# Optimization experiments

Hardware: AMD Instinct MI355X
Metric: run time of the kernel (lower is better)

## Reference

```python
import jax, jax.numpy as jnp
import numpy as np

BATCH, IN_DIM, LATENT, K = 16384, 768, 12288, 32

def setup_inputs() -> dict:
    key = jax.random.key(0)
    k1, k2, k3 = jax.random.split(key, 3)
    # kaiming-uniform-style scale for encoder/decoder weights
    enc_bound = float(np.sqrt(6.0 / IN_DIM))
    dec_bound = float(np.sqrt(6.0 / LATENT))
    x = jax.random.normal(k1, (BATCH, IN_DIM), dtype=jnp.float32)
    enc_w = jax.random.uniform(k2, (LATENT, IN_DIM), dtype=jnp.float32, minval=-enc_bound, maxval=enc_bound)
    enc_b = jnp.zeros((LATENT,), dtype=jnp.float32)
    dec_w = jax.random.uniform(k3, (IN_DIM, LATENT), dtype=jnp.float32, minval=-dec_bound, maxval=dec_bound)
    dec_b = jnp.zeros((IN_DIM,), dtype=jnp.float32)
    return {"x": x, "enc_w": enc_w, "enc_b": enc_b, "dec_w": dec_w, "dec_b": dec_b, "k": K}

def reference(x, enc_w, enc_b, dec_w, dec_b, k):
    # encode: z = x @ W_e^T + b_e            [B, LATENT]
    z = jnp.einsum('bi,li->bl', x, enc_w) + enc_b
    # top-k threshold: kth largest value per row, then shifted relu
    vals, _ = jax.lax.top_k(z, k)
    thresh = vals[:, -1:]                     # [B, 1]
    z_sparse = jax.nn.relu(z - thresh)
    # decode: dense GEMM over all latent columns (as in original module)
    x_recon = jnp.einsum('bl,il->bi', z_sparse, dec_w) + dec_b
    return (x_recon, z_sparse)
```

## Files before the change

### kernel.cpp

```cpp
#include <hip/hip_runtime.h>

#define M_DIM 16384
#define K_DIM 768
#define N_DIM 12288
#define TOPK  32
#define NCHUNK (N_DIM / 128)

typedef float f32x4 __attribute__((ext_vector_type(4)));
typedef short s16x8 __attribute__((ext_vector_type(8)));

__device__ __forceinline__ unsigned f2u(float f) {
  union { float f; unsigned u; } v; v.f = f; return v.u;
}
__device__ __forceinline__ float u2f(unsigned u) {
  union { unsigned u; float f; } v; v.u = u; return v.f;
}
__device__ __forceinline__ unsigned fkey(float f) {
  const unsigned u = f2u(f);
  return u ^ (unsigned)(((int)u >> 31) | 0x80000000);
}
__device__ __forceinline__ float kinv(unsigned k) {
  return u2f((k & 0x80000000u) ? (k ^ 0x80000000u) : ~k);
}
__device__ __forceinline__ unsigned short bf16_rne(float f) {
  unsigned u = f2u(f);
  return (unsigned short)((u + 0x7FFFu + ((u >> 16) & 1u)) >> 16);
}

__global__ __launch_bounds__(256) void TopKSparseAutoencoder_51917564674099_prep(
    const float* __restrict__ x, const float* __restrict__ w,
    const float* __restrict__ dw,
    unsigned short* __restrict__ xhi, unsigned short* __restrict__ xlo,
    unsigned short* __restrict__ whi, unsigned short* __restrict__ wlo,
    float* __restrict__ WT, int do_t, int do_s)
{
  __shared__ float tile[32][33];
  const int b = (int)blockIdx.x;
  const int t = (int)threadIdx.x;

  if (b < 9216) {
    if (!do_t) return;
    const int bx = b % (N_DIM / 32);
    const int by = b / (N_DIM / 32);
    const int tx = t & 31, ty = t >> 5;
#pragma unroll
    for (int j = 0; j < 32; j += 8)
      tile[ty + j][tx] = dw[(size_t)(by * 32 + ty + j) * N_DIM + bx * 32 + tx];
    __syncthreads();
#pragma unroll
    for (int j = 0; j < 32; j += 8)
      WT[(size_t)(bx * 32 + ty + j) * K_DIM + by * 32 + tx] = tile[tx][ty + j];
    return;
  }
  if (!do_s) return;

  const float* src; unsigned short* dh; unsigned short* dl; int i, stride, n4;
  if (b < 9216 + 1024) {
    src = x; dh = xhi; dl = xlo;
    i = (b - 9216) * 256 + t; stride = 1024 * 256; n4 = M_DIM * K_DIM / 4;
  } else {
    src = w; dh = whi; dl = wlo;
    i = (b - 10240) * 256 + t; stride = 512 * 256; n4 = N_DIM * K_DIM / 4;
  }
  for (; i < n4; i += stride) {
    const float4 v = ((const float4*)src)[i];
    ushort4 h, l;
    h.x = bf16_rne(v.x); h.y = bf16_rne(v.y); h.z = bf16_rne(v.z); h.w = bf16_rne(v.w);
    l.x = bf16_rne(v.x - u2f((unsigned)h.x << 16));
    l.y = bf16_rne(v.y - u2f((unsigned)h.y << 16));
    l.z = bf16_rne(v.z - u2f((unsigned)h.z << 16));
    l.w = bf16_rne(v.w - u2f((unsigned)h.w << 16));
    ((ushort4*)dh)[i] = h;
    ((ushort4*)dl)[i] = l;
  }
}

__device__ __forceinline__ void mfma16(f32x4& d, s16x8 a, s16x8 b) {
  asm("v_mfma_f32_16x16x32_bf16 %0, %1, %2, %0" : "+v"(d) : "v"(a), "v"(b));
}

#define GL16(g, l) __builtin_amdgcn_global_load_lds(                      \
    (const __attribute__((address_space(1))) void*)(g),                   \
    (__attribute__((address_space(3))) void*)(l), 16, 0, 0)

__global__ __launch_bounds__(256, 2) void TopKSparseAutoencoder_51917564674099_kernel(
    const unsigned short* __restrict__ Ahi, const unsigned short* __restrict__ Alo,
    const unsigned short* __restrict__ Bhi, const unsigned short* __restrict__ Blo,
    const float* __restrict__ bias, float* __restrict__ Z,
    float* __restrict__ cmax, int do_cmax)
{
  __shared__ unsigned short lds[4][128][32];
  __shared__ float cmx[128][2];

  const int t    = (int)threadIdx.x;
  const int wid  = t >> 6;
  const int lane = t & 63;

  const int bid  = (int)(blockIdx.y * gridDim.x + blockIdx.x);
  const int bswz = (bid & 7) * (12288 / 8) + (bid >> 3);
  const int n0   = (bswz % 96) * 128;
  const int m0   = (bswz / 96) * 128;

  const int rr  = lane >> 2;
  const int kq  = lane & 3;
  const int rt0 = wid * 32 + rr;
  const int rt1 = rt0 + 16;
  const int kc0 = (kq ^ ((rt0 >> 1) & 3)) * 8;
  const int kc1 = (kq ^ ((rt1 >> 1) & 3)) * 8;
  const size_t offA0 = (size_t)(m0 + rt0) * K_DIM + kc0;
  const size_t offA1 = (size_t)(m0 + rt1) * K_DIM + kc1;
  const size_t offB0 = (size_t)(n0 + rt0) * K_DIM + kc0;
  const size_t offB1 = (size_t)(n0 + rt1) * K_DIM + kc1;

  const int wm = (wid >> 1) * 64;
  const int wn = (wid & 1) * 64;
  const int lr = lane & 15;
  const int lc = lane >> 4;

  f32x4 acc[4][4];
#pragma unroll
  for (int i = 0; i < 4; ++i)
#pragma unroll
    for (int j = 0; j < 4; ++j) acc[i][j] = (f32x4){0.f, 0.f, 0.f, 0.f};

  for (int k0 = 0; k0 < K_DIM; k0 += 32) {
    GL16(Ahi + offA0 + k0, &lds[0][wid * 32][0]);
    GL16(Ahi + offA1 + k0, &lds[0][wid * 32 + 16][0]);
    GL16(Alo + offA0 + k0, &lds[1][wid * 32][0]);
    GL16(Alo + offA1 + k0, &lds[1][wid * 32 + 16][0]);
    GL16(Bhi + offB0 + k0, &lds[2][wid * 32][0]);
    GL16(Bhi + offB1 + k0, &lds[2][wid * 32 + 16][0]);
    GL16(Blo + offB0 + k0, &lds[3][wid * 32][0]);
    GL16(Blo + offB1 + k0, &lds[3][wid * 32 + 16][0]);
    __syncthreads();

    s16x8 ah[4], al[4], bh[4], bl[4];
#pragma unroll
    for (int i = 0; i < 4; ++i) {
      const int r = wm + i * 16 + lr;
      const int p = (lc ^ ((r >> 1) & 3)) * 8;
      ah[i] = *(const s16x8*)&lds[0][r][p];
      al[i] = *(const s16x8*)&lds[1][r][p];
    }
#pragma unroll
    for (int j = 0; j < 4; ++j) {
      const int r = wn + j * 16 + lr;
      const int p = (lc ^ ((r >> 1) & 3)) * 8;
      bh[j] = *(const s16x8*)&lds[2][r][p];
      bl[j] = *(const s16x8*)&lds[3][r][p];
    }
#pragma unroll
    for (int i = 0; i < 4; ++i)
#pragma unroll
      for (int j = 0; j < 4; ++j) {
        mfma16(acc[i][j], ah[i], bh[j]);
        mfma16(acc[i][j], ah[i], bl[j]);
        mfma16(acc[i][j], al[i], bh[j]);
      }
    __syncthreads();
  }

  asm volatile("s_nop 7\n\ts_nop 7" :::);

  float mx[4][4];
#pragma unroll
  for (int i = 0; i < 4; ++i)
#pragma unroll
    for (int q = 0; q < 4; ++q) mx[i][q] = -3.4e38f;

#pragma unroll
  for (int j = 0; j < 4; ++j) {
    const int col = n0 + wn + j * 16 + lr;
    const float bb = bias[col];
#pragma unroll
    for (int i = 0; i < 4; ++i) {
      const int r0 = m0 + wm + i * 16 + lc * 4;
#pragma unroll
      for (int q = 0; q < 4; ++q) {
        const float val = acc[i][j][q] + bb;
        Z[(size_t)(r0 + q) * N_DIM + col] = val;
        mx[i][q] = fmaxf(mx[i][q], val);
      }
    }
  }

  if (do_cmax) {
#pragma unroll
    for (int s = 1; s < 16; s <<= 1)
#pragma unroll
      for (int i = 0; i < 4; ++i)
#pragma unroll
        for (int q = 0; q < 4; ++q)
          mx[i][q] = fmaxf(mx[i][q], __shfl_xor(mx[i][q], s));
    if (lr == 0) {
#pragma unroll
      for (int i = 0; i < 4; ++i)
#pragma unroll
        for (int q = 0; q < 4; ++q)
          cmx[wm + i * 16 + lc * 4 + q][wid & 1] = mx[i][q];
    }
    __syncthreads();
    if (t < 128)
      cmax[(size_t)(m0 + t) * NCHUNK + (n0 >> 7)] = fmaxf(cmx[t][0], cmx[t][1]);
  }
}

__global__ void enc_gemm_f32_fb(
    const float* A, const float* B, const float* bias, float* Z)
{
  __shared__ float As[32][132];
  __shared__ float Bs[32][132];

  const int tx = (int)threadIdx.x;
  const int ty = (int)threadIdx.y;
  const int t  = ty * 16 + tx;
  const int n0 = (int)blockIdx.x * 128;
  const int m0 = (int)blockIdx.y * 128;
  const int r = t >> 1;
  const int h = (t & 1) * 16;

  float c[8][8];
#pragma unroll
  for (int i = 0; i < 8; ++i)
#pragma unroll
    for (int j = 0; j < 8; ++j) c[i][j] = 0.0f;

  for (int k0 = 0; k0 < K_DIM; k0 += 32) {
    const float* pa = A + (size_t)(m0 + r) * K_DIM + k0 + h;
    const float* pb = B + (size_t)(n0 + r) * K_DIM + k0 + h;
    float fa[16], fb[16];
#pragma unroll
    for (int j = 0; j < 16; ++j) fa[j] = pa[j];
#pragma unroll
    for (int j = 0; j < 16; ++j) fb[j] = pb[j];
#pragma unroll
    for (int j = 0; j < 16; ++j) As[h + j][r] = fa[j];
#pragma unroll
    for (int j = 0; j < 16; ++j) Bs[h + j][r] = fb[j];
    __syncthreads();

    for (int kk = 0; kk < 32; ++kk) {
      float av[8], bv[8];
#pragma unroll
      for (int i = 0; i < 8; ++i) av[i] = As[kk][ty * 8 + i];
#pragma unroll
      for (int j = 0; j < 8; ++j) bv[j] = Bs[kk][tx * 8 + j];
#pragma unroll
      for (int i = 0; i < 8; ++i)
#pragma unroll
        for (int j = 0; j < 8; ++j) c[i][j] += av[i] * bv[j];
    }
    __syncthreads();
  }

#pragma unroll
  for (int j = 0; j < 8; ++j) {
    const int col = n0 + tx * 8 + j;
    const float bb = bias[col];
#pragma unroll
    for (int i = 0; i < 8; ++i)
      Z[(size_t)(m0 + ty * 8 + i) * N_DIM + col] = c[i][j] + bb;
  }
}

__global__ __launch_bounds__(256, 4) void TopKSparseAutoencoder_51917564674099_zdecode(
    float* Z, const float* __restrict__ CMAX, const float* __restrict__ WT,
    const float* __restrict__ db, float* __restrict__ XR)
{
  __shared__ unsigned candk[512];
  __shared__ int      candi[512];
  __shared__ unsigned red[2][2][4];
  __shared__ unsigned s_B;
  __shared__ int s_cc, s_nnz;
  __shared__ int   s_col[TOPK];
  __shared__ float s_val[TOPK];

  const int row  = (int)blockIdx.x;
  const int t    = (int)threadIdx.x;
  const int lane = t & 63;
  const int wid  = t >> 6;

  if (t == 0) { s_cc = 0; s_nnz = 0; }
  if (t < TOPK) { s_col[t] = 0; s_val[t] = 0.0f; }

  if (wid == 0) {
    const unsigned kA = fkey(CMAX[(size_t)row * NCHUNK + lane]);
    const unsigned kB = (lane < NCHUNK - 64) ? fkey(CMAX[(size_t)row * NCHUNK + 64 + lane]) : 0u;
    unsigned lo = 0;
    unsigned long long w = 1ULL << 32;
    for (int r = 0; r < 8; ++r) {
      w >>= 2;
      const unsigned wu = (unsigned)w;
      const unsigned m1 = lo + wu, m2 = lo + 2u * wu, m3 = lo + 3u * wu;
      unsigned p = (unsigned)((kA >= m1) + (kB >= m1)) |
                   ((unsigned)((kA >= m2) + (kB >= m2)) << 16);
      unsigned q = (unsigned)((kA >= m3) + (kB >= m3));
      p += __shfl_down(p, 32); q += __shfl_down(q, 32);
      p += __shfl_down(p, 16); q += __shfl_down(q, 16);
      p += __shfl_down(p, 8);  q += __shfl_down(q, 8);
      p += __shfl_down(p, 4);  q += __shfl_down(q, 4);
      p += __shfl_down(p, 2);  q += __shfl_down(q, 2);
      p += __shfl_down(p, 1);  q += __shfl_down(q, 1);
      p = __shfl(p, 0); q = __shfl(q, 0);
      if (q >= (unsigned)TOPK)                  lo = m3;
      else if ((p >> 16) >= (unsigned)TOPK)     lo = m2;
      else if ((p & 0xFFFFu) >= (unsigned)TOPK) lo = m1;
    }
    if (lane == 0) s_B = lo;
  }
  __syncthreads();
  const unsigned B = s_B;

  const float4* zr = (const float4*)(Z + (size_t)row * N_DIM);
#pragma unroll
  for (int j = 0; j < 12; ++j) {
    const float4 v = zr[t + 256 * j];
    const int base = (t + 256 * j) * 4;
    const unsigned k0 = fkey(v.x), k1 = fkey(v.y), k2 = fkey(v.z), k3 = fkey(v.w);
    if (k0 >= B) { int p = atomicAdd(&s_cc, 1); if (p < 512) { candk[p] = k0; candi[p] = base; } }
    if (k1 >= B) { int p = atomicAdd(&s_cc, 1); if (p < 512) { candk[p] = k1; candi[p] = base + 1; } }
    if (k2 >= B) { int p = atomicAdd(&s_cc, 1); if (p < 512) { candk[p] = k2; candi[p] = base + 2; } }
    if (k3 >= B) { int p = atomicAdd(&s_cc, 1); if (p < 512) { candk[p] = k3; candi[p] = base + 3; } }
  }
  __syncthreads();
  const int cc = s_cc;
  float4* zw = (float4*)(Z + (size_t)row * N_DIM);

  if (cc <= 512) {
    if (wid == 0) {
      unsigned k[8];
#pragma unroll
      for (int i = 0; i < 8; ++i) k[i] = (lane + 64 * i < cc) ? candk[lane + 64 * i] : 0u;
      unsigned lo = 0;
      unsigned long long w = 1ULL << 32;
      for (int r = 0; r < 16; ++r) {
        w >>= 2;
        const unsigned wu = (unsigned)w;
        const unsigned m1 = lo + wu, m2 = lo + 2u * wu, m3 = lo + 3u * wu;
        unsigned c1 = 0, c2 = 0, c3 = 0;
#pragma unroll
        for (int i = 0; i < 8; ++i) {
          c1 += (k[i] >= m1); c2 += (k[i] >= m2); c3 += (k[i] >= m3);
        }
        unsigned p = c1 | (c2 << 16), q = c3;
        p += __shfl_down(p, 32); q += __shfl_down(q, 32);
        p += __shfl_down(p, 16); q += __shfl_down(q, 16);
        p += __shfl_down(p, 8);  q += __shfl_down(q, 8);
        p += __shfl_down(p, 4);  q += __shfl_down(q, 4);
        p += __shfl_down(p, 2);  q += __shfl_down(q, 2);
        p += __shfl_down(p, 1);  q += __shfl_down(q, 1);
        p = __shfl(p, 0); q = __shfl(q, 0);
        if (q >= (unsigned)TOPK)                  lo = m3;
        else if ((p >> 16) >= (unsigned)TOPK)     lo = m2;
        else if ((p & 0xFFFFu) >= (unsigned)TOPK) lo = m1;
      }
      const unsigned T = lo;
      const float thresh = kinv(T);
      for (int i = lane; i < cc; i += 64) {
        const unsigned ck = candk[i];
        if (ck > T) {
          const int p = atomicAdd(&s_nnz, 1);
          if (p < TOPK) { s_col[p] = candi[i]; s_val[p] = kinv(ck) - thresh; }
        }
      }
    } else {
      const float4 z4 = {0.f, 0.f, 0.f, 0.f};
#pragma unroll
      for (int jj = 0; jj < 16; ++jj)
        zw[(wid - 1) * 64 + lane + 192 * jj] = z4;
    }
    __syncthreads();
  } else {
    unsigned lo = 0;
    unsigned long long w = 1ULL << 32;
    for (int r = 0; r < 16; ++r) {
      w >>= 2;
      const unsigned wu = (unsigned)w;
      const unsigned m1 = lo + wu, m2 = lo + 2u * wu, m3 = lo + 3u * wu;
      unsigned c1 = 0, c2 = 0, c3 = 0;
      for (int j = 0; j < 12; ++j) {
        const float4 v = zr[t + 256 * j];
        const unsigned k0 = fkey(v.x), k1 = fkey(v.y), k2 = fkey(v.z), k3 = fkey(v.w);
        c1 += (k0 >= m1) + (k1 >= m1) + (k2 >= m1) + (k3 >= m1);
        c2 += (k0 >= m2) + (k1 >= m2) + (k2 >= m2) + (k3 >= m2);
        c3 += (k0 >= m3) + (k1 >= m3) + (k2 >= m3) + (k3 >= m3);
      }
      unsigned p = c1 | (c2 << 16), q = c3;
      p += __shfl_down(p, 32); q += __shfl_down(q, 32);
      p += __shfl_down(p, 16); q += __shfl_down(q, 16);
      p += __shfl_down(p, 8);  q += __shfl_down(q, 8);
      p += __shfl_down(p, 4);  q += __shfl_down(q, 4);
      p += __shfl_down(p, 2);  q += __shfl_down(q, 2);
      p += __shfl_down(p, 1);  q += __shfl_down(q, 1);
      const int par = r & 1;
      if (lane == 0) { red[par][0][wid] = p; red[par][1][wid] = q; }
      __syncthreads();
      const unsigned P = red[par][0][0] + red[par][0][1] + red[par][0][2] + red[par][0][3];
      const unsigned Q = red[par][1][0] + red[par][1][1] + red[par][1][2] + red[par][1][3];
      if (Q >= (unsigned)TOPK)                  lo = m3;
      else if ((P >> 16) >= (unsigned)TOPK)     lo = m2;
      else if ((P & 0xFFFFu) >= (unsigned)TOPK) lo = m1;
    }
    const unsigned T = lo;
    const float thresh = kinv(T);
    const float4 z4 = {0.f, 0.f, 0.f, 0.f};
    for (int j = 0; j < 12; ++j) {
      const float4 v = zr[t + 256 * j];
      const int base = (t + 256 * j) * 4;
      const unsigned k0 = fkey(v.x), k1 = fkey(v.y), k2 = fkey(v.z), k3 = fkey(v.w);
      if (k0 > T) { int p = atomicAdd(&s_nnz, 1); if (p < TOPK) { s_col[p] = base;     s_val[p] = kinv(k0) - thresh; } }
      if (k1 > T) { int p = atomicAdd(&s_nnz, 1); if (p < TOPK) { s_col[p] = base + 1; s_val[p] = kinv(k1) - thresh; } }
      if (k2 > T) { int p = atomicAdd(&s_nnz, 1); if (p < TOPK) { s_col[p] = base + 2; s_val[p] = kinv(k2) - thresh; } }
      if (k3 > T) { int p = atomicAdd(&s_nnz, 1); if (p < TOPK) { s_col[p] = base + 3; s_val[p] = kinv(k3) - thresh; } }
      zw[t + 256 * j] = z4;
    }
    __syncthreads();
  }

  const int nnz = (s_nnz < TOPK) ? s_nnz : TOPK;
  if (t < nnz) Z[(size_t)row * N_DIM + s_col[t]] = s_val[t];

  float a0 = 0.0f, a1 = 0.0f, a2 = 0.0f;
#pragma unroll 8
  for (int j = 0; j < TOPK; ++j) {
    const float v = s_val[j];
    const float* wp = WT + (size_t)s_col[j] * K_DIM;
    a0 += v * wp[t];
    a1 += v * wp[t + 256];
    a2 += v * wp[t + 512];
  }
  float* xr = XR + (size_t)row * K_DIM;
  xr[t]       = a0 + db[t];
  xr[t + 256] = a1 + db[t + 256];
  xr[t + 512] = a2 + db[t + 512];
}

__device__ __forceinline__ void full_round_l(
    const uint4* zk, unsigned red[][2][4], int t, int lane, int wid, int r,
    unsigned& lo, unsigned long long& w)
{
  w >>= 2;
  const unsigned wu = (unsigned)w;
  const unsigned m1 = lo + wu, m2 = lo + 2u * wu, m3 = lo + 3u * wu;
  unsigned c1 = 0, c2 = 0, c3 = 0;
#pragma unroll
  for (int j = 0; j < 12; ++j) {
    const uint4 k = zk[t + 256 * j];
    c1 += (k.x >= m1) + (k.y >= m1) + (k.z >= m1) + (k.w >= m1);
    c2 += (k.x >= m2) + (k.y >= m2) + (k.z >= m2) + (k.w >= m2);
    c3 += (k.x >= m3) + (k.y >= m3) + (k.z >= m3) + (k.w >= m3);
  }
  unsigned p = c1 | (c2 << 16), q = c3;
  p += __shfl_down(p, 32); q += __shfl_down(q, 32);
  p += __shfl_down(p, 16); q += __shfl_down(q, 16);
  p += __shfl_down(p, 8);  q += __shfl_down(q, 8);
  p += __shfl_down(p, 4);  q += __shfl_down(q, 4);
  p += __shfl_down(p, 2);  q += __shfl_down(q, 2);
  p += __shfl_down(p, 1);  q += __shfl_down(q, 1);
  const int par = r & 1;
  if (lane == 0) { red[par][0][wid] = p; red[par][1][wid] = q; }
  __syncthreads();
  const unsigned P = red[par][0][0] + red[par][0][1] + red[par][0][2] + red[par][0][3];
  const unsigned Q = red[par][1][0] + red[par][1][1] + red[par][1][2] + red[par][1][3];
  if (Q >= (unsigned)TOPK)                lo = m3;
  else if ((P >> 16) >= (unsigned)TOPK)   lo = m2;
  else if ((P & 0xFFFFu) >= (unsigned)TOPK) lo = m1;
}

__global__ __launch_bounds__(256, 3) void topk_select_decode_fb(
    float* Z, const float* __restrict__ WT, const float* __restrict__ DW,
    const float* __restrict__ db, float* __restrict__ XR, int use_wt)
{
  __shared__ uint4 zkey4[N_DIM / 4];
  __shared__ unsigned red[2][2][4];
  __shared__ unsigned cand[256];
  __shared__ unsigned s_T;
  __shared__ int s_cc;
  __shared__ int s_nnz;
  __shared__ int   s_col[TOPK];
  __shared__ float s_val[TOPK];

  const int row  = (int)blockIdx.x;
  const int t    = (int)threadIdx.x;
  const int lane = t & 63;
  const int wid  = t >> 6;

  float4* zv = (float4*)(Z + (size_t)row * N_DIM);

#pragma unroll
  for (int j = 0; j < 12; ++j) {
    const float4 v = zv[t + 256 * j];
    uint4 k;
    k.x = fkey(v.x); k.y = fkey(v.y); k.z = fkey(v.z); k.w = fkey(v.w);
    zkey4[t + 256 * j] = k;
  }
  if (t == 0) { s_nnz = 0; s_cc = 0; }
  if (t < TOPK) { s_col[t] = 0; s_val[t] = 0.0f; }
  __syncthreads();

  unsigned lo = 0;
  unsigned long long w = 1ULL << 32;
  for (int r = 0; r < 8; ++r)
    full_round_l(zkey4, red, t, lane, wid, r, lo, w);

#pragma unroll
  for (int j = 0; j < 12; ++j) {
    const uint4 k = zkey4[t + 256 * j];
    if (k.x >= lo) { int p = atomicAdd(&s_cc, 1); if (p < 256) cand[p] = k.x; }
    if (k.y >= lo) { int p = atomicAdd(&s_cc, 1); if (p < 256) cand[p] = k.y; }
    if (k.z >= lo) { int p = atomicAdd(&s_cc, 1); if (p < 256) cand[p] = k.z; }
    if (k.w >= lo) { int p = atomicAdd(&s_cc, 1); if (p < 256) cand[p] = k.w; }
  }
  __syncthreads();
  const int cc = s_cc;

  if (cc <= 256) {
    if (wid == 0) {
      const unsigned k0 = (lane       < cc) ? cand[lane]       : 0u;
      const unsigned k1 = (lane + 64  < cc) ? cand[lane + 64]  : 0u;
      const unsigned k2 = (lane + 128 < cc) ? cand[lane + 128] : 0u;
      const unsigned k3 = (lane + 192 < cc) ? cand[lane + 192] : 0u;
      for (int r = 8; r < 16; ++r) {
        w >>= 2;
        const unsigned wu = (unsigned)w;
        const unsigned m1 = lo + wu, m2 = lo + 2u * wu, m3 = lo + 3u * wu;
        unsigned c1 = (k0 >= m1) + (k1 >= m1) + (k2 >= m1) + (k3 >= m1);
        unsigned c2 = (k0 >= m2) + (k1 >= m2) + (k2 >= m2) + (k3 >= m2);
        unsigned c3 = (k0 >= m3) + (k1 >= m3) + (k2 >= m3) + (k3 >= m3);
        unsigned p = c1 | (c2 << 16), q = c3;
        p += __shfl_down(p, 32); q += __shfl_down(q, 32);
        p += __shfl_down(p, 16); q += __shfl_down(q, 16);
        p += __shfl_down(p, 8);  q += __shfl_down(q, 8);
        p += __shfl_down(p, 4);  q += __shfl_down(q, 4);
        p += __shfl_down(p, 2);  q += __shfl_down(q, 2);
        p += __shfl_down(p, 1);  q += __shfl_down(q, 1);
        p = __shfl(p, 0); q = __shfl(q, 0);
        if (q >= (unsigned)TOPK)                  lo = m3;
        else if ((p >> 16) >= (unsigned)TOPK)     lo = m2;
        else if ((p & 0xFFFFu) >= (unsigned)TOPK) lo = m1;
      }
      if (lane == 0) s_T = lo;
    }
  } else {
    for (int r = 8; r < 16; ++r)
      full_round_l(zkey4, red, t, lane, wid, r, lo, w);
    if (t == 0) s_T = lo;
  }
  __syncthreads();
  const unsigned T = s_T;
  const float thresh = kinv(T);

#define COMPF(KF, OFS, OF) {                                                  \
      float v = 0.0f;                                                         \
      if (KF > T) {                                                           \
        v = kinv(KF) - thresh;                                                \
        const int p = atomicAdd(&s_nnz, 1);                                   \
        if (p < TOPK) { s_col[p] = base + OFS; s_val[p] = v; }                \
      }                                                                       \
      o.OF = v; }
#pragma unroll
  for (int j = 0; j < 12; ++j) {
    const uint4 k = zkey4[t + 256 * j];
    const int base = (t + 256 * j) * 4;
    float4 o;
    COMPF(k.x, 0, x)
    COMPF(k.y, 1, y)
    COMPF(k.z, 2, z)
    COMPF(k.w, 3, w)
    zv[t + 256 * j] = o;
  }
#undef COMPF
  __syncthreads();

  float a0 = 0.0f, a1 = 0.0f, a2 = 0.0f;
  if (use_wt) {
#pragma unroll 8
    for (int j = 0; j < TOPK; ++j) {
      const float v = s_val[j];
      const float* wp = WT + (size_t)s_col[j] * K_DIM;
      a0 += v * wp[t];
      a1 += v * wp[t + 256];
      a2 += v * wp[t + 512];
    }
  } else {
#pragma unroll 8
    for (int j = 0; j < TOPK; ++j) {
      const float v = s_val[j];
      const int col = s_col[j];
      a0 += v * DW[(size_t)(t)       * N_DIM + col];
      a1 += v * DW[(size_t)(t + 256) * N_DIM + col];
      a2 += v * DW[(size_t)(t + 512) * N_DIM + col];
    }
  }
  float* xr = XR + (size_t)row * K_DIM;
  xr[t]       = a0 + db[t];
  xr[t + 256] = a1 + db[t + 256];
  xr[t + 512] = a2 + db[t + 512];
}

extern "C" void kernel_launch(void* const* d_in, const int* in_sizes, int n_in,
                              void* d_out, int out_size, void* d_ws, size_t ws_size,
                              hipStream_t stream)
{
  (void)in_sizes; (void)n_in; (void)out_size;

  const float* x     = (const float*)d_in[0];
  const float* enc_w = (const float*)d_in[1];
  const float* enc_b = (const float*)d_in[2];
  const float* dec_w = (const float*)d_in[3];
  const float* dec_b = (const float*)d_in[4];

  float* out     = (float*)d_out;
  float* x_recon = out;
  float* z_sp    = out + (size_t)M_DIM * K_DIM;

  const size_t WT_BYTES = (size_t)N_DIM * K_DIM * sizeof(float);
  const size_t XPLANE   = (size_t)M_DIM * K_DIM * sizeof(unsigned short);
  const size_t WPLANE   = (size_t)N_DIM * K_DIM * sizeof(unsigned short);
  const size_t FULL     = WT_BYTES + 2 * XPLANE + 2 * WPLANE;
  const size_t CMAX_B   = (size_t)M_DIM * NCHUNK * sizeof(float);
  const size_t FULL2    = FULL + CMAX_B;

  char* ws = (char*)d_ws;
  const int use_wt   = (ws_size >= WT_BYTES) ? 1 : 0;
  const int use_mfma = (ws_size >= FULL) ? 1 : 0;
  const int use_cmax = (ws_size >= FULL2) ? 1 : 0;

  float*          WT   = (float*)ws;
  unsigned short* xhi  = (unsigned short*)(ws + WT_BYTES);
  unsigned short* xlo  = (unsigned short*)(ws + WT_BYTES + XPLANE);
  unsigned short* whi  = (unsigned short*)(ws + WT_BYTES + 2 * XPLANE);
  unsigned short* wlo  = (unsigned short*)(ws + WT_BYTES + 2 * XPLANE + WPLANE);
  float*          CMAX = (float*)(ws + FULL);

  if (use_wt || use_mfma)
    TopKSparseAutoencoder_51917564674099_prep<<<10752, 256, 0, stream>>>(
        x, enc_w, dec_w, xhi, xlo, whi, wlo, WT, use_wt, use_mfma);

  if (use_mfma) {
    dim3 tg(N_DIM / 128, M_DIM / 128);
    TopKSparseAutoencoder_51917564674099_kernel<<<tg, 256, 0, stream>>>(
        xhi, xlo, whi, wlo, enc_b, z_sp, CMAX, use_cmax);
  } else {
    dim3 tb(16, 16);
    dim3 tg(N_DIM / 128, M_DIM / 128);
    enc_gemm_f32_fb<<<tg, tb, 0, stream>>>(x, enc_w, enc_b, z_sp);
  }

  if (use_cmax)
    TopKSparseAutoencoder_51917564674099_zdecode<<<M_DIM, 256, 0, stream>>>(
        z_sp, CMAX, WT, dec_b, x_recon);
  else
    topk_select_decode_fb<<<M_DIM, 256, 0, stream>>>(
        z_sp, WT, dec_w, dec_b, x_recon, use_wt);
}
```

Baseline: 2.232 ms.

## Double-buffer GEMM LDS loads and scan only eligible chunks in top-k

The encoder GEMM now uses two LDS buffers: it prefetches the next K-slice with global_load_lds while MFMAs run on the current one, which removes one barrier per iteration. The top-k candidate pass now reads only the 128-column chunks whose max reaches the threshold, done by wave 0, instead of streaming the whole Z row across all 256 threads. LDS per GEMM block doubles, which may cut occupancy from 2 blocks/CU. The candidate scan becomes single-wave, and the zdecode launch-bounds hint is loosened. The prefetch issued before the compute reads is protected only by the trailing barrier, so ordering depends on the async LDS writes finishing correctly.

New measurement: 2.249 ms. Within noise of the previous version (+0.8%).

```diff
diff --git a/kernel.cpp b/kernel.cpp
--- a/kernel.cpp
+++ b/kernel.cpp
@@ -89,7 +89,7 @@
     const float* __restrict__ bias, float* __restrict__ Z,
     float* __restrict__ cmax, int do_cmax)
 {
-  __shared__ unsigned short lds[4][128][32];
+  __shared__ unsigned short lds[2][4][128][32];
   __shared__ float cmx[128][2];
 
   const int t    = (int)threadIdx.x;
@@ -123,31 +123,38 @@
 #pragma unroll
     for (int j = 0; j < 4; ++j) acc[i][j] = (f32x4){0.f, 0.f, 0.f, 0.f};
 
+#define STAGE(B, KOFF) do {                                          \
+    GL16(Ahi + offA0 + (KOFF), &lds[B][0][wid * 32][0]);             \
+    GL16(Ahi + offA1 + (KOFF), &lds[B][0][wid * 32 + 16][0]);        \
+    GL16(Alo + offA0 + (KOFF), &lds[B][1][wid * 32][0]);             \
+    GL16(Alo + offA1 + (KOFF), &lds[B][1][wid * 32 + 16][0]);        \
+    GL16(Bhi + offB0 + (KOFF), &lds[B][2][wid * 32][0]);             \
+    GL16(Bhi + offB1 + (KOFF), &lds[B][2][wid * 32 + 16][0]);        \
+    GL16(Blo + offB0 + (KOFF), &lds[B][3][wid * 32][0]);             \
+    GL16(Blo + offB1 + (KOFF), &lds[B][3][wid * 32 + 16][0]);        \
+  } while (0)
+
+  STAGE(0, 0);
+  __syncthreads();
+
+  int cur = 0;
   for (int k0 = 0; k0 < K_DIM; k0 += 32) {
-    GL16(Ahi + offA0 + k0, &lds[0][wid * 32][0]);
-    GL16(Ahi + offA1 + k0, &lds[0][wid * 32 + 16][0]);
-    GL16(Alo + offA0 + k0, &lds[1][wid * 32][0]);
-    GL16(Alo + offA1 + k0, &lds[1][wid * 32 + 16][0]);
-    GL16(Bhi + offB0 + k0, &lds[2][wid * 32][0]);
-    GL16(Bhi + offB1 + k0, &lds[2][wid * 32 + 16][0]);
-    GL16(Blo + offB0 + k0, &lds[3][wid * 32][0]);
-    GL16(Blo + offB1 + k0, &lds[3][wid * 32 + 16][0]);
-    __syncthreads();
+    if (k0 + 32 < K_DIM) STAGE(cur ^ 1, k0 + 32);
 
     s16x8 ah[4], al[4], bh[4], bl[4];
 #pragma unroll
     for (int i = 0; i < 4; ++i) {
       const int r = wm + i * 16 + lr;
       const int p = (lc ^ ((r >> 1) & 3)) * 8;
-      ah[i] = *(const s16x8*)&lds[0][r][p];
-      al[i] = *(const s16x8*)&lds[1][r][p];
+      ah[i] = *(const s16x8*)&lds[cur][0][r][p];
+      al[i] = *(const s16x8*)&lds[cur][1][r][p];
     }
 #pragma unroll
     for (int j = 0; j < 4; ++j) {
       const int r = wn + j * 16 + lr;
       const int p = (lc ^ ((r >> 1) & 3)) * 8;
-      bh[j] = *(const s16x8*)&lds[2][r][p];
-      bl[j] = *(const s16x8*)&lds[3][r][p];
+      bh[j] = *(const s16x8*)&lds[cur][2][r][p];
+      bl[j] = *(const s16x8*)&lds[cur][3][r][p];
     }
 #pragma unroll
     for (int i = 0; i < 4; ++i)
@@ -158,7 +165,9 @@
         mfma16(acc[i][j], al[i], bh[j]);
       }
     __syncthreads();
-  }
+    cur ^= 1;
+  }
+#undef STAGE
 
   asm volatile("s_nop 7\n\ts_nop 7" :::);
 
@@ -263,15 +272,15 @@
   }
 }
 
-__global__ __launch_bounds__(256, 4) void TopKSparseAutoencoder_51917564674099_zdecode(
+__global__ __launch_bounds__(256) void TopKSparseAutoencoder_51917564674099_zdecode(
     float* Z, const float* __restrict__ CMAX, const float* __restrict__ WT,
     const float* __restrict__ db, float* __restrict__ XR)
 {
   __shared__ unsigned candk[512];
   __shared__ int      candi[512];
+  __shared__ int      s_elig[NCHUNK];
   __shared__ unsigned red[2][2][4];
-  __shared__ unsigned s_B;
-  __shared__ int s_cc, s_nnz;
+  __shared__ int s_ne, s_cc, s_nnz;
   __shared__ int   s_col[TOPK];
   __shared__ float s_val[TOPK];
 
@@ -280,12 +289,15 @@
   const int lane = t & 63;
   const int wid  = t >> 6;
 
-  if (t == 0) { s_cc = 0; s_nnz = 0; }
+  if (t == 0) { s_ne = 0; s_cc = 0; s_nnz = 0; }
   if (t < TOPK) { s_col[t] = 0; s_val[t] = 0.0f; }
+
+  const float4* zr = (const float4*)(Z + (size_t)row * N_DIM);
 
   if (wid == 0) {
     const unsigned kA = fkey(CMAX[(size_t)row * NCHUNK + lane]);
     const unsigned kB = (lane < NCHUNK - 64) ? fkey(CMAX[(size_t)row * NCHUNK + 64 + lane]) : 0u;
+
     unsigned lo = 0;
     unsigned long long w = 1ULL << 32;
     for (int r = 0; r < 8; ++r) {
@@ -306,21 +318,22 @@
       else if ((p >> 16) >= (unsigned)TOPK)     lo = m2;
       else if ((p & 0xFFFFu) >= (unsigned)TOPK) lo = m1;
     }
-    if (lane == 0) s_B = lo;
-  }
-  __syncthreads();
-  const unsigned B = s_B;
-
-  const float4* zr = (const float4*)(Z + (size_t)row * N_DIM);
-#pragma unroll
-  for (int j = 0; j < 12; ++j) {
-    const float4 v = zr[t + 256 * j];
-    const int base = (t + 256 * j) * 4;
-    const unsigned k0 = fkey(v.x), k1 = fkey(v.y), k2 = fkey(v.z), k3 = fkey(v.w);
-    if (k0 >= B) { int p = atomicAdd(&s_cc, 1); if (p < 512) { candk[p] = k0; candi[p] = base; } }
-    if (k1 >= B) { int p = atomicAdd(&s_cc, 1); if (p < 512) { candk[p] = k1; candi[p] = base + 1; } }
-    if (k2 >= B) { int p = atomicAdd(&s_cc, 1); if (p < 512) { candk[p] = k2; candi[p] = base + 2; } }
-    if (k3 >= B) { int p = atomicAdd(&s_cc, 1); if (p < 512) { candk[p] = k3; candi[p] = base + 3; } }
+    const unsigned B = lo;
+
+    if (kA >= B) { const int p = atomicAdd(&s_ne, 1); s_elig[p] = lane; }
+    if (lane < NCHUNK - 64 && kB >= B) { const int p = atomicAdd(&s_ne, 1); s_elig[p] = lane + 64; }
+    const int ne = __shfl(s_ne, 0);
+    for (int i = (lane >> 5); i < ne; i += 2) {
+      const int c  = s_elig[i];
+      const int f4 = (c << 5) + (lane & 31);
+      const float4 v = zr[f4];
+      const int base = f4 << 2;
+      const unsigned k0 = fkey(v.x), k1 = fkey(v.y), k2 = fkey(v.z), k3 = fkey(v.w);
+      if (k0 >= B) { int p = atomicAdd(&s_cc, 1); if (p < 512) { candk[p] = k0; candi[p] = base; } }
+      if (k1 >= B) { int p = atomicAdd(&s_cc, 1); if (p < 512) { candk[p] = k1; candi[p] = base + 1; } }
+      if (k2 >= B) { int p = atomicAdd(&s_cc, 1); if (p < 512) { candk[p] = k2; candi[p] = base + 2; } }
+      if (k3 >= B) { int p = atomicAdd(&s_cc, 1); if (p < 512) { candk[p] = k3; candi[p] = base + 3; } }
+    }
   }
   __syncthreads();
   const int cc = s_cc;
```

## Process one row per wavefront and scan only eligible chunks in top-k decode

Applied to the files above, without the earlier changes.

The top-k/decode kernel now maps one row to each 64-lane wavefront (four rows per block) instead of one row per block, which removes the block-wide barriers. Using the per-chunk maxima, each wave collects the chunks whose max reaches the coarse bound and rereads only those 128-column chunks of Z to gather candidates, rather than scanning the whole row. The decode gather switches to 16-byte vector loads of WT rows, and a vmcnt wait orders the zeroing stores before the sparse value writes. The trade-off is less parallelism per row: each wave issues all 48 zeroing stores for its row, and the fallback path now does its full-row counting passes on a single wave.

Result: faster. 2.170 ms (-2.8%).

```diff
diff --git a/kernel.cpp b/kernel.cpp
--- a/kernel.cpp
+++ b/kernel.cpp
@@ -267,34 +267,84 @@
     float* Z, const float* __restrict__ CMAX, const float* __restrict__ WT,
     const float* __restrict__ db, float* __restrict__ XR)
 {
-  __shared__ unsigned candk[512];
-  __shared__ int      candi[512];
-  __shared__ unsigned red[2][2][4];
-  __shared__ unsigned s_B;
-  __shared__ int s_cc, s_nnz;
-  __shared__ int   s_col[TOPK];
-  __shared__ float s_val[TOPK];
-
-  const int row  = (int)blockIdx.x;
+  __shared__ unsigned candk[4][256];
+  __shared__ int      candi[4][256];
+  __shared__ short    s_elig[4][NCHUNK];
+  __shared__ int s_ne[4], s_cc[4], s_nnz[4];
+  __shared__ int   s_col[4][TOPK];
+  __shared__ float s_val[4][TOPK];
+
   const int t    = (int)threadIdx.x;
   const int lane = t & 63;
   const int wid  = t >> 6;
-
-  if (t == 0) { s_cc = 0; s_nnz = 0; }
-  if (t < TOPK) { s_col[t] = 0; s_val[t] = 0.0f; }
-
-  if (wid == 0) {
-    const unsigned kA = fkey(CMAX[(size_t)row * NCHUNK + lane]);
-    const unsigned kB = (lane < NCHUNK - 64) ? fkey(CMAX[(size_t)row * NCHUNK + 64 + lane]) : 0u;
-    unsigned lo = 0;
-    unsigned long long w = 1ULL << 32;
-    for (int r = 0; r < 8; ++r) {
+  const int row  = (int)blockIdx.x * 4 + wid;
+
+  if (lane == 0) { s_ne[wid] = 0; s_cc[wid] = 0; s_nnz[wid] = 0; }
+  if (lane < TOPK) { s_col[wid][lane] = 0; s_val[wid][lane] = 0.0f; }
+
+  const f32x4* zr = (const f32x4*)(Z + (size_t)row * N_DIM);
+  f32x4*       zw = (f32x4*)(Z + (size_t)row * N_DIM);
+
+  const unsigned kA = fkey(CMAX[(size_t)row * NCHUNK + lane]);
+  const unsigned kB = (lane < NCHUNK - 64) ? fkey(CMAX[(size_t)row * NCHUNK + 64 + lane]) : 0u;
+  unsigned lo = 0;
+  unsigned long long w = 1ULL << 32;
+  for (int r = 0; r < 8; ++r) {
+    w >>= 2;
+    const unsigned wu = (unsigned)w;
+    const unsigned m1 = lo + wu, m2 = lo + 2u * wu, m3 = lo + 3u * wu;
+    unsigned p = (unsigned)((kA >= m1) + (kB >= m1)) |
+                 ((unsigned)((kA >= m2) + (kB >= m2)) << 16);
+    unsigned q = (unsigned)((kA >= m3) + (kB >= m3));
+    p += __shfl_down(p, 32); q += __shfl_down(q, 32);
+    p += __shfl_down(p, 16); q += __shfl_down(q, 16);
+    p += __shfl_down(p, 8);  q += __shfl_down(q, 8);
+    p += __shfl_down(p, 4);  q += __shfl_down(q, 4);
+    p += __shfl_down(p, 2);  q += __shfl_down(q, 2);
+    p += __shfl_down(p, 1);  q += __shfl_down(q, 1);
+    p = __shfl(p, 0); q = __shfl(q, 0);
+    if (q >= (unsigned)TOPK)                  lo = m3;
+    else if ((p >> 16) >= (unsigned)TOPK)     lo = m2;
+    else if ((p & 0xFFFFu) >= (unsigned)TOPK) lo = m1;
+  }
+  const unsigned B = lo;
+
+  if (kA >= B) { const int p = atomicAdd(&s_ne[wid], 1); s_elig[wid][p] = (short)lane; }
+  if (lane < NCHUNK - 64 && kB >= B) {
+    const int p = atomicAdd(&s_ne[wid], 1); s_elig[wid][p] = (short)(lane + 64);
+  }
+  const int ne = s_ne[wid];
+
+  for (int i = (lane >> 5); i < ne; i += 2) {
+    const int c  = (int)s_elig[wid][i];
+    const int f4 = (c << 5) + (lane & 31);
+    const f32x4 v = zr[f4];
+    const int base = f4 << 2;
+    const unsigned k0 = fkey(v[0]), k1 = fkey(v[1]), k2 = fkey(v[2]), k3 = fkey(v[3]);
+    if (k0 >= B) { int p = atomicAdd(&s_cc[wid], 1); if (p < 256) { candk[wid][p] = k0; candi[wid][p] = base; } }
+    if (k1 >= B) { int p = atomicAdd(&s_cc[wid], 1); if (p < 256) { candk[wid][p] = k1; candi[wid][p] = base + 1; } }
+    if (k2 >= B) { int p = atomicAdd(&s_cc[wid], 1); if (p < 256) { candk[wid][p] = k2; candi[wid][p] = base + 2; } }
+    if (k3 >= B) { int p = atomicAdd(&s_cc[wid], 1); if (p < 256) { candk[wid][p] = k3; candi[wid][p] = base + 3; } }
+  }
+  const int cc = s_cc[wid];
+  const f32x4 z4 = (f32x4){0.f, 0.f, 0.f, 0.f};
+
+  if (cc <= 256) {
+#pragma unroll 8
+    for (int jj = 0; jj < 48; ++jj) zw[lane + 64 * jj] = z4;
+
+    unsigned k[4];
+#pragma unroll
+    for (int i = 0; i < 4; ++i) k[i] = (lane + 64 * i < cc) ? candk[wid][lane + 64 * i] : 0u;
+    lo = 0; w = 1ULL << 32;
+    for (int r = 0; r < 16; ++r) {
       w >>= 2;
       const unsigned wu = (unsigned)w;
       const unsigned m1 = lo + wu, m2 = lo + 2u * wu, m3 = lo + 3u * wu;
-      unsigned p = (unsigned)((kA >= m1) + (kB >= m1)) |
-                   ((unsigned)((kA >= m2) + (kB >= m2)) << 16);
-      unsigned q = (unsigned)((kA >= m3) + (kB >= m3));
+      unsigned c1 = 0, c2 = 0, c3 = 0;
+#pragma unroll
+      for (int i = 0; i < 4; ++i) { c1 += (k[i] >= m1); c2 += (k[i] >= m2); c3 += (k[i] >= m3); }
+      unsigned p = c1 | (c2 << 16), q = c3;
       p += __shfl_down(p, 32); q += __shfl_down(q, 32);
       p += __shfl_down(p, 16); q += __shfl_down(q, 16);
       p += __shfl_down(p, 8);  q += __shfl_down(q, 8);
@@ -306,81 +356,25 @@
       else if ((p >> 16) >= (unsigned)TOPK)     lo = m2;
       else if ((p & 0xFFFFu) >= (unsigned)TOPK) lo = m1;
     }
-    if (lane == 0) s_B = lo;
-  }
-  __syncthreads();
-  const unsigned B = s_B;
-
-  const float4* zr = (const float4*)(Z + (size_t)row * N_DIM);
-#pragma unroll
-  for (int j = 0; j < 12; ++j) {
-    const float4 v = zr[t + 256 * j];
-    const int base = (t + 256 * j) * 4;
-    const unsigned k0 = fkey(v.x), k1 = fkey(v.y), k2 = fkey(v.z), k3 = fkey(v.w);
-    if (k0 >= B) { int p = atomicAdd(&s_cc, 1); if (p < 512) { candk[p] = k0; candi[p] = base; } }
-    if (k1 >= B) { int p = atomicAdd(&s_cc, 1); if (p < 512) { candk[p] = k1; candi[p] = base + 1; } }
-    if (k2 >= B) { int p = atomicAdd(&s_cc, 1); if (p < 512) { candk[p] = k2; candi[p] = base + 2; } }
-    if (k3 >= B) { int p = atomicAdd(&s_cc, 1); if (p < 512) { candk[p] = k3; candi[p] = base + 3; } }
-  }
-  __syncthreads();
-  const int cc = s_cc;
-  float4* zw = (float4*)(Z + (size_t)row * N_DIM);
-
-  if (cc <= 512) {
-    if (wid == 0) {
-      unsigned k[8];
-#pragma unroll
-      for (int i = 0; i < 8; ++i) k[i] = (lane + 64 * i < cc) ? candk[lane + 64 * i] : 0u;
-      unsigned lo = 0;
-      unsigned long long w = 1ULL << 32;
-      for (int r = 0; r < 16; ++r) {
-        w >>= 2;
-        const unsigned wu = (unsigned)w;
-        const unsigned m1 = lo + wu, m2 = lo + 2u * wu, m3 = lo + 3u * wu;
-        unsigned c1 = 0, c2 = 0, c3 = 0;
-#pragma unroll
-        for (int i = 0; i < 8; ++i) {
-          c1 += (k[i] >= m1); c2 += (k[i] >= m2); c3 += (k[i] >= m3);
-        }
-        unsigned p = c1 | (c2 << 16), q = c3;
-        p += __shfl_down(p, 32); q += __shfl_down(q, 32);
-        p += __shfl_down(p, 16); q += __shfl_down(q, 16);
-        p += __shfl_down(p, 8);  q += __shfl_down(q, 8);
-        p += __shfl_down(p, 4);  q += __shfl_down(q, 4);
-        p += __shfl_down(p, 2);  q += __shfl_down(q, 2);
-        p += __shfl_down(p, 1);  q += __shfl_down(q, 1);
-        p = __shfl(p, 0); q = __shfl(q, 0);
-        if (q >= (unsigned)TOPK)                  lo = m3;
-        else if ((p >> 16) >= (unsigned)TOPK)     lo = m2;
-        else if ((p & 0xFFFFu) >= (unsigned)TOPK) lo = m1;
+    const unsigned T = lo;
+    const float thresh = kinv(T);
+    for (int i = lane; i < cc; i += 64) {
+      const unsigned ck = candk[wid][i];
+      if (ck > T) {
+        const int p = atomicAdd(&s_nnz[wid], 1);
+        if (p < TOPK) { s_col[wid][p] = candi[wid][i]; s_val[wid][p] = kinv(ck) - thresh; }
       }
-      const unsigned T = lo;
-      const float thresh = kinv(T);
-      for (int i = lane; i < cc; i += 64) {
-        const unsigned ck = candk[i];
-        if (ck > T) {
-          const int p = atomicAdd(&s_nnz, 1);
-          if (p < TOPK) { s_col[p] = candi[i]; s_val[p] = kinv(ck) - thresh; }
-        }
-      }
-    } else {
-      const float4 z4 = {0.f, 0.f, 0.f, 0.f};
-#pragma unroll
-      for (int jj = 0; jj < 16; ++jj)
-        zw[(wid - 1) * 64 + lane + 192 * jj] = z4;
-    }
-    __syncthreads();
+    }
   } else {
-    unsigned lo = 0;
-    unsigned long long w = 1ULL << 32;
+    lo = 0; w = 1ULL << 32;
     for (int r = 0; r < 16; ++r) {
       w >>= 2;
       const unsigned wu = (unsigned)w;
       const unsigned m1 = lo + wu, m2 = lo + 2u * wu, m3 = lo + 3u * wu;
       unsigned c1 = 0, c2 = 0, c3 = 0;
-      for (int j = 0; j < 12; ++j) {
-        const float4 v = zr[t + 256 * j];
-        const unsigned k0 = fkey(v.x), k1 = fkey(v.y), k2 = fkey(v.z), k3 = fkey(v.w);
+      for (int j = 0; j < 48; ++j) {
+        const f32x4 v = zr[lane + 64 * j];
+        const unsigned k0 = fkey(v[0]), k1 = fkey(v[1]), k2 = fkey(v[2]), k3 = fkey(v[3]);
         c1 += (k0 >= m1) + (k1 >= m1) + (k2 >= m1) + (k3 >= m1);
         c2 += (k0 >= m2) + (k1 >= m2) + (k2 >= m2) + (k3 >= m2);
         c3 += (k0 >= m3) + (k1 >= m3) + (k2 >= m3) + (k3 >= m3);
@@ -392,47 +386,47 @@
       p += __shfl_down(p, 4);  q += __shfl_down(q, 4);
       p += __shfl_down(p, 2);  q += __shfl_down(q, 2);
       p += __shfl_down(p, 1);  q += __shfl_down(q, 1);
-      const int par = r & 1;
-      if (lane == 0) { red[par][0][wid] = p; red[par][1][wid] = q; }
-      __syncthreads();
-      const unsigned P = red[par][0][0] + red[par][0][1] + red[par][0][2] + red[par][0][3];
-      const unsigned Q = red[par][1][0] + red[par][1][1] + red[par][1][2] + red[par][1][3];
-      if (Q >= (unsigned)TOPK)                  lo = m3;
-      else if ((P >> 16) >= (unsigned)TOPK)     lo = m2;
-      else if ((P & 0xFFFFu) >= (unsigned)TOPK) lo = m1;
+      p = __shfl(p, 0); q = __shfl(q, 0);
+      if (q >= (unsigned)TOPK)                  lo = m3;
+      else if ((p >> 16) >= (unsigned)TOPK)     lo = m2;
+      else if ((p & 0xFFFFu) >= (unsigned)TOPK) lo = m1;
     }
     const unsigned T = lo;
     const float thresh = kinv(T);
-    const float4 z4 = {0.f, 0.f, 0.f, 0.f};
-    for (int j = 0; j < 12; ++j) {
-      const float4 v = zr[t + 256 * j];
-      const int base = (t + 256 * j) * 4;
-      const unsigned k0 = fkey(v.x), k1 = fkey(v.y), k2 = fkey(v.z), k3 = fkey(v.w);
-      if (k0 > T) { int p = atomicAdd(&s_nnz, 1); if (p < TOPK) { s_col[p] = base;     s_val[p] = kinv(k0) - thresh; } }
-      if (k1 > T) { int p = atomicAdd(&s_nnz, 1); if (p < TOPK) { s_col[p] = base + 1; s_val[p] = kinv(k1) - thresh; } }
-      if (k2 > T) { int p = atomicAdd(&s_nnz, 1); if (p < TOPK) { s_col[p] = base + 2; s_val[p] = kinv(k2) - thresh; } }
-      if (k3 > T) { int p = atomicAdd(&s_nnz, 1); if (p < TOPK) { s_col[p] = base + 3; s_val[p] = kinv(k3) - thresh; } }
-      zw[t + 256 * j] = z4;
-    }
-    __syncthreads();
-  }
-
-  const int nnz = (s_nnz < TOPK) ? s_nnz : TOPK;
-  if (t < nnz) Z[(size_t)row * N_DIM + s_col[t]] = s_val[t];
-
-  float a0 = 0.0f, a1 = 0.0f, a2 = 0.0f;
-#pragma unroll 8
+    for (int j = 0; j < 48; ++j) {
+      const f32x4 v = zr[lane + 64 * j];
+      const int base = (lane + 64 * j) * 4;
+      const unsigned k0 = fkey(v[0]), k1 = fkey(v[1]), k2 = fkey(v[2]), k3 = fkey(v[3]);
+      if (k0 > T) { int p = atomicAdd(&s_nnz[wid], 1); if (p < TOPK) { s_col[wid][p] = base;     s_val[wid][p] = kinv(k0) - thresh; } }
+      if (k1 > T) { int p = atomicAdd(&s_nnz[wid], 1); if (p < TOPK) { s_col[wid][p] = base + 1; s_val[wid][p] = kinv(k1) - thresh; } }
+      if (k2 > T) { int p = atomicAdd(&s_nnz[wid], 1); if (p < TOPK) { s_col[wid][p] = base + 2; s_val[wid][p] = kinv(k2) - thresh; } }
+      if (k3 > T) { int p = atomicAdd(&s_nnz[wid], 1); if (p < TOPK) { s_col[wid][p] = base + 3; s_val[wid][p] = kinv(k3) - thresh; } }
+      zw[lane + 64 * j] = z4;
+    }
+  }
+
+  asm volatile("s_waitcnt vmcnt(0)" ::: "memory");
+  const int nnz = (s_nnz[wid] < TOPK) ? s_nnz[wid] : TOPK;
+  if (lane < nnz) Z[(size_t)row * N_DIM + s_col[wid][lane]] = s_val[wid][lane];
+
+  const f32x4* WT4 = (const f32x4*)WT;
+  f32x4 a0 = z4, a1 = z4, a2 = z4;
+#pragma unroll 4
   for (int j = 0; j < TOPK; ++j) {
-    const float v = s_val[j];
-    const float* wp = WT + (size_t)s_col[j] * K_DIM;
-    a0 += v * wp[t];
-    a1 += v * wp[t + 256];
-    a2 += v * wp[t + 512];
-  }
-  float* xr = XR + (size_t)row * K_DIM;
-  xr[t]       = a0 + db[t];
-  xr[t + 256] = a1 + db[t + 256];
-  xr[t + 512] = a2 + db[t + 512];
+    const float v = s_val[wid][j];
+    const size_t base = (size_t)s_col[wid][j] * (K_DIM / 4);
+    const f32x4 w0 = WT4[base + lane];
+    const f32x4 w1 = WT4[base + 64 + lane];
+    const f32x4 w2 = WT4[base + 128 + lane];
+    a0 += w0 * v;
+    a1 += w1 * v;
+    a2 += w2 * v;
+  }
+  const f32x4* db4 = (const f32x4*)db;
+  f32x4* xr4 = (f32x4*)(XR + (size_t)row * K_DIM);
+  xr4[lane]        = a0 + db4[lane];
+  xr4[64 + lane]   = a1 + db4[64 + lane];
+  xr4[128 + lane]  = a2 + db4[128 + lane];
 }
 
 __device__ __forceinline__ void full_round_l(
@@ -648,7 +642,7 @@
   }
 
   if (use_cmax)
-    TopKSparseAutoencoder_51917564674099_zdecode<<<M_DIM, 256, 0, stream>>>(
+    TopKSparseAutoencoder_51917564674099_zdecode<<<M_DIM / 4, 256, 0, stream>>>(
         z_sp, CMAX, WT, dec_b, x_recon);
   else
     topk_select_decode_fb<<<M_DIM, 256, 0, stream>>>(
```
